# Kernel tuning notes

Measured on AMD Instinct MI355X. Metric: run time of the kernel, lower is better.

Reference implementation:

```python
import jax, jax.numpy as jnp
import numpy as np

B, D, H, C, K = 16384, 128, 4, 64, 16  # nodes, feat dim, heads, out per head, top-k
NEG_SLOPE = 0.2
NEG_INF = -1e9


def setup_inputs() -> dict:
    key = jax.random.key(0)
    ks = jax.random.split(key, 7)
    s = 1.0 / np.sqrt(D)
    return {
        "x": jax.random.normal(ks[0], (B, D), jnp.float32),
        "W_l": jax.random.normal(ks[1], (D, H * C), jnp.float32) * s,
        "b_l": jnp.zeros((H * C,), jnp.float32),
        "W_r": jax.random.normal(ks[2], (D, H * C), jnp.float32) * s,
        "b_r": jnp.zeros((H * C,), jnp.float32),
        "att": jax.random.normal(ks[3], (H, C), jnp.float32) * (1.0 / np.sqrt(C)),
        "bias": jnp.zeros((H * C,), jnp.float32),
        "k": K,
    }


def reference(x, W_l, b_l, W_r, b_r, att, bias, k):
    Bn, Dn = x.shape
    scale = 1.0 / np.sqrt(Dn)
    # dense similarity + top-k graph build (softmax is monotone, so top-k of
    # scaled logits equals top-k of softmax probs)
    attn = (x @ x.T) * scale                      # [B, B]
    _, idx = jax.lax.top_k(attn, k)               # [B, k]

    # edges: node b -> its top-k similar nodes (adj[b, idx[b]] = 1)
    src = jnp.repeat(jnp.arange(Bn), k)           # [B*k]
    dst = idx.reshape(-1)                          # [B*k]
    # GATv2Conv removes self loops then adds exactly one per node
    valid = src != dst
    self_idx = jnp.arange(Bn)
    src = jnp.concatenate([src, self_idx])
    dst = jnp.concatenate([dst, self_idx])
    valid = jnp.concatenate([valid, jnp.ones((Bn,), bool)])  # [E], E = B*(k+1)

    # GATv2: x_l = lin_l(x) for source, x_r = lin_r(x) for target
    x_l = (x @ W_l + b_l).reshape(Bn, H, C)
    x_r = (x @ W_r + b_r).reshape(Bn, H, C)

    msg = x_l[src]                                 # [E, H, C] source features
    s = jax.nn.leaky_relu(msg + x_r[dst], NEG_SLOPE)
    score = jnp.einsum('ehc,hc->eh', s, att)       # [E, H]
    score = jnp.where(valid[:, None], score, NEG_INF)

    # segment softmax over edges grouped by target node
    m = jax.ops.segment_max(score, dst, num_segments=Bn)        # [B, H]
    ex = jnp.exp(score - m[dst]) * valid[:, None].astype(score.dtype)
    denom = jax.ops.segment_sum(ex, dst, num_segments=Bn)       # [B, H]
    alpha = ex / denom[dst]                                     # [E, H]

    out = jax.ops.segment_sum(alpha[:, :, None] * msg, dst, num_segments=Bn)
    return out.reshape(Bn, H * C) + bias
```

## Files before the change

kernel.cpp:

```cpp
#include <hip/hip_runtime.h>
#include <math.h>

#define BN 16384
#define DK 128
#define HN 4
#define CN 64
#define HC 256
#define TK 16
#define CAP 512

#define GSPLIT 16
#define GSPAN  1024
#define GBC    128
#define GNT    (GSPAN / GBC)

#define NSTRIP 2
#define SCOLS (BN / NSTRIP)
#define RPB 64
#define CT 64

typedef float4 f4;
typedef __attribute__((ext_vector_type(8))) short short8;
typedef __attribute__((ext_vector_type(4))) float f32x4;

__device__ __forceinline__ unsigned bf_rne(float f) {
  unsigned u = __float_as_uint(f);
  u += 0x7fffu + ((u >> 16) & 1u);
  return u >> 16;
}

__device__ __forceinline__ unsigned fmap(float f) {
  unsigned b = __float_as_uint(f);
  return (b & 0x80000000u) ? ~b : (b | 0x80000000u);
}

__device__ __forceinline__ void gload16(const unsigned short* g,
                                        unsigned short* l) {
  __builtin_amdgcn_global_load_lds(
      (const __attribute__((address_space(1))) unsigned int*)g,
      (__attribute__((address_space(3))) unsigned int*)l, 16, 0, 0);
}

__global__ __launch_bounds__(256) void k_init(int* deg, int* cur,
                                              unsigned* gmaxu) {
  int i = blockIdx.x * 256 + threadIdx.x;
  if (i < BN) { deg[i] = 1; cur[i] = 0; }
  if (i < BN * 16) gmaxu[i] = 0u;
}

__global__ __launch_bounds__(256) void k_lin(const float* __restrict__ x,
    const float* __restrict__ Wl, const float* __restrict__ bl,
    const float* __restrict__ Wr, const float* __restrict__ br,
    float* __restrict__ xl, float* __restrict__ xr) {
  __shared__ __align__(16) float xst[DK][16];
  int tid = threadIdx.x;
  int r0 = blockIdx.x * 16;
  for (int i = 0; i < 2; ++i) {
    int s = tid + i * 256;
    int r = s >> 5, kq = s & 31;
    f4 v = *(const f4*)&x[(size_t)(r0 + r) * DK + kq * 4];
    xst[kq*4+0][r] = v.x; xst[kq*4+1][r] = v.y;
    xst[kq*4+2][r] = v.z; xst[kq*4+3][r] = v.w;
  }
  __syncthreads();
  float al[16], ar[16];
  #pragma unroll
  for (int r = 0; r < 16; ++r) { al[r] = 0.f; ar[r] = 0.f; }
  for (int k = 0; k < DK; ++k) {
    float wl = Wl[k * HC + tid];
    float wr = Wr[k * HC + tid];
    float xv[16];
    *(f4*)&xv[0]  = *(const f4*)&xst[k][0];
    *(f4*)&xv[4]  = *(const f4*)&xst[k][4];
    *(f4*)&xv[8]  = *(const f4*)&xst[k][8];
    *(f4*)&xv[12] = *(const f4*)&xst[k][12];
    #pragma unroll
    for (int r = 0; r < 16; ++r) { al[r] += xv[r] * wl; ar[r] += xv[r] * wr; }
  }
  float bbl = bl[tid], bbr = br[tid];
  #pragma unroll
  for (int r = 0; r < 16; ++r) {
    xl[(size_t)(r0 + r) * HC + tid] = al[r] + bbl;
    xr[(size_t)(r0 + r) * HC + tid] = ar[r] + bbr;
  }
}

__global__ __launch_bounds__(256) void k_cvt(const float* __restrict__ x,
                                             unsigned short* __restrict__ xbf) {
  size_t base = (size_t)(blockIdx.x * 256 + threadIdx.x) * 8;
  f4 a = *(const f4*)&x[base];
  f4 b = *(const f4*)&x[base + 4];
  uint4 o;
  o.x = bf_rne(a.x) | (bf_rne(a.y) << 16);
  o.y = bf_rne(a.z) | (bf_rne(a.w) << 16);
  o.z = bf_rne(b.x) | (bf_rne(b.y) << 16);
  o.w = bf_rne(b.z) | (bf_rne(b.w) << 16);
  *(uint4*)&xbf[base] = o;
}

template <int MODE>
__global__ __launch_bounds__(512) void k_gemm_t(
    const unsigned short* __restrict__ xbf, unsigned* __restrict__ gmaxu,
    const unsigned* __restrict__ tau_u, int* __restrict__ cnt,
    int* __restrict__ cand) {
  __shared__ __align__(16) unsigned short As[128 * DK];
  __shared__ __align__(16) unsigned short Bs0[128 * DK];
  __shared__ __align__(16) unsigned short Bs1[128 * DK];
  __shared__ float red[4][128];
  int tid = threadIdx.x;
  int q0 = blockIdx.y * 128;
  int c0 = blockIdx.x * GSPAN;
  int lane = tid & 63;
  int wid = tid >> 6;
  int wm = wid & 1, wn = wid >> 1;
  int tq = lane & 15, th = lane >> 4;

  int soff[4];
  #pragma unroll
  for (int i = 0; i < 4; ++i) {
    int slot = tid + i * 512;
    int row = slot >> 4, c8 = slot & 15;
    soff[i] = row * DK + ((c8 ^ (row & 7)) * 8);
  }
  #pragma unroll
  for (int i = 0; i < 4; ++i)
    gload16(&xbf[(size_t)q0 * DK + soff[i]], &As[(tid + i * 512) * 8]);
  #pragma unroll
  for (int i = 0; i < 4; ++i)
    gload16(&xbf[(size_t)c0 * DK + soff[i]], &Bs0[(tid + i * 512) * 8]);
  __syncthreads();

  short8 af[4][4];
  #pragma unroll
  for (int m = 0; m < 4; ++m) {
    int ra = 64 * wm + 16 * m + tq;
    #pragma unroll
    for (int ks = 0; ks < 4; ++ks)
      af[m][ks] = *(const short8*)&As[ra * DK + (((ks*4+th) ^ (ra & 7)) * 8)];
  }

  float gmx[4][4];
  float tauf[4][4];
  if constexpr (MODE == 0) {
    #pragma unroll
    for (int m = 0; m < 4; ++m)
      #pragma unroll
      for (int r = 0; r < 4; ++r) gmx[m][r] = -3.0e38f;
  } else {
    #pragma unroll
    for (int m = 0; m < 4; ++m)
      #pragma unroll
      for (int r = 0; r < 4; ++r) {
        unsigned tu = tau_u[q0 + 64*wm + 16*m + 4*th + r];
        tauf[m][r] = __uint_as_float(
            (tu >= 0x80000000u) ? (tu ^ 0x80000000u) : ~tu);
      }
  }

  if constexpr (MODE == 0) {
    unsigned short* Bc = Bs0;
    unsigned short* Bn = Bs1;
    for (int t = 0; t < GNT; ++t) {
      if (t + 1 < GNT) {
        size_t gb = (size_t)(c0 + (t + 1) * GBC) * DK;
        #pragma unroll
        for (int i = 0; i < 4; ++i)
          gload16(&xbf[gb + soff[i]], &Bn[(tid + i * 512) * 8]);
      }
      short8 bfr[2][4];
      #pragma unroll
      for (int n = 0; n < 2; ++n) {
        int rb = 32 * wn + 16 * n + tq;
        #pragma unroll
        for (int ks = 0; ks < 4; ++ks)
          bfr[n][ks] = *(const short8*)&Bc[rb * DK +
                          (((ks*4+th) ^ (rb & 7)) * 8)];
      }
      f32x4 acc[4][2];
      #pragma unroll
      for (int m = 0; m < 4; ++m)
        #pragma unroll
        for (int n = 0; n < 2; ++n) {
          acc[m][n][0] = 0.f; acc[m][n][1] = 0.f;
          acc[m][n][2] = 0.f; acc[m][n][3] = 0.f;
        }
      #pragma unroll
      for (int ks = 0; ks < 4; ++ks)
        #pragma unroll
        for (int m = 0; m < 4; ++m)
          #pragma unroll
          for (int n = 0; n < 2; ++n)
            acc[m][n] = __builtin_amdgcn_mfma_f32_16x16x32_bf16(
                af[m][ks], bfr[n][ks], acc[m][n], 0, 0, 0);
      #pragma unroll
      for (int m = 0; m < 4; ++m)
        #pragma unroll
        for (int r = 0; r < 4; ++r)
          gmx[m][r] = fmaxf(gmx[m][r], fmaxf(acc[m][0][r], acc[m][1][r]));
      __syncthreads();
      unsigned short* tb = Bc; Bc = Bn; Bn = tb;
    }
    #pragma unroll
    for (int m = 0; m < 4; ++m)
      #pragma unroll
      for (int r = 0; r < 4; ++r) {
        float v = gmx[m][r];
        #pragma unroll
        for (int w = 1; w < 16; w <<= 1) v = fmaxf(v, __shfl_xor(v, w, 64));
        if (tq == 0) red[wn][64*wm + 16*m + 4*th + r] = v;
      }
    __syncthreads();
    if (tid < 128) {
      float v = fmaxf(fmaxf(red[0][tid], red[1][tid]),
                      fmaxf(red[2][tid], red[3][tid]));
      gmaxu[(q0 + tid) * 16 + blockIdx.x] = fmap(v);
    }
  } else {
    unsigned hm[GNT];
    #pragma unroll
    for (int i = 0; i < GNT; ++i) hm[i] = 0u;
    #pragma unroll
    for (int t = 0; t < GNT; ++t) {
      unsigned short* Bc = (t & 1) ? Bs1 : Bs0;
      unsigned short* Bn = (t & 1) ? Bs0 : Bs1;
      if (t + 1 < GNT) {
        size_t gb = (size_t)(c0 + (t + 1) * GBC) * DK;
        #pragma unroll
        for (int i = 0; i < 4; ++i)
          gload16(&xbf[gb + soff[i]], &Bn[(tid + i * 512) * 8]);
      }
      short8 bfr[2][4];
      #pragma unroll
      for (int n = 0; n < 2; ++n) {
        int rb = 32 * wn + 16 * n + tq;
        #pragma unroll
        for (int ks = 0; ks < 4; ++ks)
          bfr[n][ks] = *(const short8*)&Bc[rb * DK +
                          (((ks*4+th) ^ (rb & 7)) * 8)];
      }
      f32x4 acc[4][2];
      #pragma unroll
      for (int m = 0; m < 4; ++m)
        #pragma unroll
        for (int n = 0; n < 2; ++n) {
          acc[m][n][0] = 0.f; acc[m][n][1] = 0.f;
          acc[m][n][2] = 0.f; acc[m][n][3] = 0.f;
        }
      #pragma unroll
      for (int ks = 0; ks < 4; ++ks)
        #pragma unroll
        for (int m = 0; m < 4; ++m)
          #pragma unroll
          for (int n = 0; n < 2; ++n)
            acc[m][n] = __builtin_amdgcn_mfma_f32_16x16x32_bf16(
                af[m][ks], bfr[n][ks], acc[m][n], 0, 0, 0);
      unsigned mm = 0;
      #pragma unroll
      for (int m = 0; m < 4; ++m)
        #pragma unroll
        for (int r = 0; r < 4; ++r)
          #pragma unroll
          for (int n = 0; n < 2; ++n)
            mm |= (acc[m][n][r] >= tauf[m][r])
                      ? (1u << ((m << 3) | (r << 1) | n)) : 0u;
      hm[t] = mm;
      __syncthreads();
    }
    #pragma unroll
    for (int t = 0; t < GNT; ++t) {
      unsigned mm = hm[t];
      while (mm) {
        int b = __ffs(mm) - 1;
        mm &= mm - 1;
        int m = b >> 3, r = (b >> 1) & 3, n = b & 1;
        int row = q0 + 64*wm + 16*m + 4*th + r;
        int col = c0 + t * GBC + 32*wn + 16*n + tq;
        int slot = atomicAdd(&cnt[row], 1);
        if (slot < CAP) cand[(size_t)row * CAP + slot] = col;
      }
    }
  }
}

__global__ __launch_bounds__(256) void k_tau(const unsigned* __restrict__ gmaxu,
    unsigned* __restrict__ tau_u, int* __restrict__ cnt) {
  int row = blockIdx.x * 256 + threadIdx.x;
  unsigned t = 0xFFFFFFFFu;
  #pragma unroll
  for (int g = 0; g < 16; ++g) t = min(t, gmaxu[row * 16 + g]);
  tau_u[row] = t;
  cnt[row] = 0;
}

__global__ __launch_bounds__(256, 4) void k_exact(const float* __restrict__ x,
    const int* __restrict__ cand, const int* __restrict__ cnt,
    int* __restrict__ idx) {
  __shared__ __align__(16) float arow[4][DK];
  int lane = threadIdx.x & 63, wid = threadIdx.x >> 6;
  int row = blockIdx.x * 4 + wid;
  int n = cnt[row];
  if (lane < 32)
    *(f4*)&arow[wid][lane * 4] = *(const f4*)&x[(size_t)row * DK + lane * 4];
  __syncthreads();
  if (n > CAP) return;
  const f4* as = (const f4*)&arow[wid][0];

  if (n <= 64) {
    bool ok = lane < n;
    int col = ok ? cand[(size_t)row * CAP + lane] : row;
    const f4* b4 = (const f4*)&x[(size_t)col * DK];
    f4 pre[8];
    #pragma unroll
    for (int q = 0; q < 8; ++q) pre[q] = b4[q * 4];
    float t = 0.f;
    #pragma unroll
    for (int k = 0; k < 32; ++k) {
      f4 a = as[k];
      f4 b = ((k & 3) == 0) ? pre[k >> 2] : b4[k];
      t = fmaf(a.x, b.x, t); t = fmaf(a.y, b.y, t);
      t = fmaf(a.z, b.z, t); t = fmaf(a.w, b.w, t);
    }
    float sv = ok ? t : -3.0e38f;
    int cc = ok ? col : 0x7fffffff;
    int rk = 0;
    for (int l = 0; l < 64; ++l) {
      float vj = __shfl(sv, l, 64);
      int   cj = __shfl(cc, l, 64);
      rk += (vj > sv || (vj == sv && cj < cc)) ? 1 : 0;
    }
    if (ok && rk < TK) idx[(size_t)row * TK + rk] = cc;
  } else {
    int NCH = (n + 63) >> 6;
    float sv[8]; int cc[8]; int rk[8];
    #pragma unroll
    for (int p = 0; p < 8; ++p) {
      sv[p] = -3.0e38f; cc[p] = 0x7fffffff; rk[p] = 0;
    }
    #pragma unroll
    for (int p = 0; p < 8; ++p) {
      if (p < NCH) {
        int i = p * 64 + lane;
        bool ok = i < n;
        int col = ok ? cand[(size_t)row * CAP + i] : row;
        const f4* b4 = (const f4*)&x[(size_t)col * DK];
        f4 pre[8];
        #pragma unroll
        for (int q = 0; q < 8; ++q) pre[q] = b4[q * 4];
        float t = 0.f;
        #pragma unroll
        for (int k = 0; k < 32; ++k) {
          f4 a = as[k];
          f4 b = ((k & 3) == 0) ? pre[k >> 2] : b4[k];
          t = fmaf(a.x, b.x, t); t = fmaf(a.y, b.y, t);
          t = fmaf(a.z, b.z, t); t = fmaf(a.w, b.w, t);
        }
        if (ok) { sv[p] = t; cc[p] = col; }
      }
    }
    #pragma unroll
    for (int q = 0; q < 8; ++q) {
      if (q < NCH) {
        for (int l = 0; l < 64; ++l) {
          float vj = __shfl(sv[q], l, 64);
          int   cj = __shfl(cc[q], l, 64);
          #pragma unroll
          for (int p = 0; p < 8; ++p)
            rk[p] += (vj > sv[p] || (vj == sv[p] && cj < cc[p])) ? 1 : 0;
        }
      }
    }
    #pragma unroll
    for (int p = 0; p < 8; ++p) {
      int i = p * 64 + lane;
      if (p < NCH && i < n && rk[p] < TK) idx[(size_t)row * TK + rk[p]] = cc[p];
    }
  }
}

__global__ __launch_bounds__(256) void k_exact_of(const float* __restrict__ x,
    const int* __restrict__ cnt, int* __restrict__ idx) {
  int lane = threadIdx.x & 63, wid = threadIdx.x >> 6;
  int row = blockIdx.x * 4 + wid;
  if (cnt[row] <= CAP) return;
  const f4* a4 = (const f4*)&x[(size_t)row * DK];
  float bv[16]; int bc[16];
  #pragma unroll
  for (int i = 0; i < 16; ++i) { bv[i] = -3.0e38f; bc[i] = 0x7fffffff; }
  for (int c = lane; c < BN; c += 64) {
    const f4* b4 = (const f4*)&x[(size_t)c * DK];
    float s = 0.f;
    #pragma unroll
    for (int k = 0; k < 32; ++k) {
      f4 a = a4[k], b = b4[k];
      s = fmaf(a.x, b.x, s); s = fmaf(a.y, b.y, s);
      s = fmaf(a.z, b.z, s); s = fmaf(a.w, b.w, s);
    }
    if (s > bv[15] || (s == bv[15] && c < bc[15])) {
      bv[15] = s; bc[15] = c;
      #pragma unroll
      for (int i = 15; i > 0; --i) {
        bool sw = bv[i] > bv[i-1] || (bv[i] == bv[i-1] && bc[i] < bc[i-1]);
        if (sw) {
          float tv = bv[i]; bv[i] = bv[i-1]; bv[i-1] = tv;
          int tc = bc[i]; bc[i] = bc[i-1]; bc[i-1] = tc;
        }
      }
    }
  }
  for (int t = 0; t < TK; ++t) {
    float mv = bv[0]; int mc = bc[0];
    #pragma unroll
    for (int w = 1; w < 64; w <<= 1) {
      float ov = __shfl_xor(mv, w, 64);
      int   oc = __shfl_xor(mc, w, 64);
      if (ov > mv || (ov == mv && oc < mc)) { mv = ov; mc = oc; }
    }
    if (bv[0] == mv && bc[0] == mc) {
      idx[(size_t)row * TK + t] = mc;
      #pragma unroll
      for (int i = 0; i < 15; ++i) { bv[i] = bv[i+1]; bc[i] = bc[i+1]; }
      bv[15] = -3.0e38f; bc[15] = 0x7fffffff;
    }
  }
}

__global__ __launch_bounds__(256) void k_sim(const float* __restrict__ x,
    int* __restrict__ candC) {
  __shared__ __align__(16) float At[DK][RPB];
  __shared__ __align__(16) float Bt[CT][DK];
  int tid = threadIdx.x;
  int rowblk = blockIdx.x & 255;
  int strip  = blockIdx.x >> 8;
  int r0 = rowblk * RPB;
  int tx = tid & 15, ty = tid >> 4;
  int lane = tid & 63;
  int gbase = lane & 48;
  for (int i = 0; i < 8; ++i) {
    int s = tid + i * 256;
    int r = s >> 5, kq = s & 31;
    f4 v = *(const f4*)&x[(size_t)(r0 + r) * DK + kq * 4];
    At[kq*4+0][r] = v.x; At[kq*4+1][r] = v.y;
    At[kq*4+2][r] = v.z; At[kq*4+3][r] = v.w;
  }
  float listV[4]; int listC[4];
  #pragma unroll
  for (int rr = 0; rr < 4; ++rr) { listV[rr] = -3.0e38f; listC[rr] = 0; }
  __syncthreads();
  for (int ct = 0; ct < SCOLS / CT; ++ct) {
    int c0 = strip * SCOLS + ct * CT;
    for (int i = 0; i < 8; ++i) {
      int s = tid + i * 256;
      int c = s >> 5, kq = s & 31;
      f4 v = *(const f4*)&x[(size_t)(c0 + c) * DK + kq * 4];
      ((f4*)&Bt[c][0])[kq ^ (c & 7)] = v;
    }
    __syncthreads();
    float acc[4][4];
    #pragma unroll
    for (int a = 0; a < 4; ++a)
      #pragma unroll
      for (int b = 0; b < 4; ++b) acc[a][b] = 0.f;
    #pragma unroll 2
    for (int k4 = 0; k4 < 32; ++k4) {
      float ta[4][4], tb[4][4];
      #pragma unroll
      for (int j = 0; j < 4; ++j)
        *(f4*)&ta[j][0] = *(const f4*)&At[k4*4 + j][ty*4];
      #pragma unroll
      for (int jj = 0; jj < 4; ++jj) {
        int c = tx + 16*jj;
        *(f4*)&tb[jj][0] = ((const f4*)&Bt[c][0])[k4 ^ (c & 7)];
      }
      #pragma unroll
      for (int rr = 0; rr < 4; ++rr)
        #pragma unroll
        for (int jj = 0; jj < 4; ++jj)
          acc[rr][jj] += ta[0][rr]*tb[jj][0] + ta[1][rr]*tb[jj][1]
                       + ta[2][rr]*tb[jj][2] + ta[3][rr]*tb[jj][3];
    }
    float tau[4];
    #pragma unroll
    for (int rr = 0; rr < 4; ++rr) tau[rr] = __shfl(listV[rr], 15, 16);
    #pragma unroll
    for (int rr = 0; rr < 4; ++rr) {
      #pragma unroll
      for (int jj = 0; jj < 4; ++jj) {
        float v = acc[rr][jj];
        unsigned long long bal = __ballot(v > tau[rr]);
        unsigned bits = (unsigned)((bal >> gbase) & 0xffffULL);
        while (bits) {
          int l = __ffs(bits) - 1;
          float vb = __shfl(v, l, 16);
          int colb = c0 + l + 16*jj;
          unsigned long long g2 = __ballot(listV[rr] > vb);
          int cnt2 = __popc((unsigned)((g2 >> gbase) & 0xffffULL));
          float sV = __shfl_up(listV[rr], 1, 16);
          int   sC = __shfl_up(listC[rr], 1, 16);
          if (tx == cnt2)      { listV[rr] = vb; listC[rr] = colb; }
          else if (tx > cnt2)  { listV[rr] = sV; listC[rr] = sC; }
          bits &= bits - 1;
        }
      }
    }
    __syncthreads();
  }
  #pragma unroll
  for (int rr = 0; rr < 4; ++rr) {
    int row = r0 + ty * 4 + rr;
    candC[row * (NSTRIP * TK) + strip * TK + tx] = listC[rr];
  }
}

__global__ __launch_bounds__(256) void k_rescore(const float* __restrict__ x,
    const int* __restrict__ candC, int* __restrict__ idx) {
  int lane = threadIdx.x & 63;
  int wid  = threadIdx.x >> 6;
  int half = lane >> 5;
  int ci   = lane & 31;
  int row  = (blockIdx.x * 4 + wid) * 2 + half;
  int col  = candC[row * (NSTRIP * TK) + ci];
  const f4* a4 = (const f4*)&x[(size_t)row * DK];
  const f4* b4 = (const f4*)&x[(size_t)col * DK];
  float s = 0.f;
  #pragma unroll
  for (int k = 0; k < 32; ++k) {
    f4 a = a4[k], b = b4[k];
    s = fmaf(a.x, b.x, s);
    s = fmaf(a.y, b.y, s);
    s = fmaf(a.z, b.z, s);
    s = fmaf(a.w, b.w, s);
  }
  int rank = 0;
  #pragma unroll
  for (int j = 0; j < 32; ++j) {
    float vj = __shfl(s, j, 32);
    int   cj = __shfl(col, j, 32);
    if (vj > s || (vj == s && cj < col)) rank++;
  }
  if (rank < TK) idx[row * TK + rank] = col;
}

__global__ __launch_bounds__(256) void k_count(const int* __restrict__ idx,
                                               int* __restrict__ deg) {
  int i = blockIdx.x * 256 + threadIdx.x;
  int b = i >> 4;
  int t = idx[i];
  if (t != b) atomicAdd(&deg[t], 1);
}

__global__ __launch_bounds__(1024) void k_scan(const int* __restrict__ deg,
                                               int* __restrict__ off) {
  __shared__ int sdat[1024];
  int tid = threadIdx.x;
  int carry = 0;
  for (int ch = 0; ch < BN / 1024; ++ch) {
    int i = ch * 1024 + tid;
    int v = deg[i];
    sdat[tid] = v;
    __syncthreads();
    for (int o = 1; o < 1024; o <<= 1) {
      int t = (tid >= o) ? sdat[tid - o] : 0;
      __syncthreads();
      sdat[tid] += t;
      __syncthreads();
    }
    off[i] = sdat[tid] - v + carry;
    int tot = sdat[1023];
    __syncthreads();
    carry += tot;
  }
  if (tid == 0) off[BN] = carry;
}

__global__ __launch_bounds__(256) void k_fill(const int* __restrict__ idx,
    const int* __restrict__ off, int* __restrict__ cur, int* __restrict__ csr) {
  int i = blockIdx.x * 256 + threadIdx.x;
  if (i >= BN * (TK + 1)) return;
  int b = i / (TK + 1);
  int j = i - b * (TK + 1);
  int t;
  if (j < TK) { t = idx[b * TK + j]; if (t == b) return; }
  else t = b;
  int p = atomicAdd(&cur[t], 1);
  csr[off[t] + p] = b;
}

__global__ __launch_bounds__(256) void k_aggr(const float* __restrict__ xl,
    const float* __restrict__ xr, const float* __restrict__ att,
    const float* __restrict__ bias, const int* __restrict__ off,
    const int* __restrict__ csr, float* __restrict__ out) {
  int t = blockIdx.x;
  int tid = threadIdx.x;
  int o0 = off[t], o1 = off[t + 1];
  float xrv = xr[(size_t)t * HC + tid];
  float av = att[tid];
  float m = -3.0e38f, den = 0.f, acc = 0.f;
  for (int e = o0; e < o1; ++e) {
    int s = csr[e];
    float xlv = xl[(size_t)s * HC + tid];
    float z = xlv + xrv;
    z = (z > 0.f) ? z : 0.2f * z;
    float sc = z * av;
    #pragma unroll
    for (int w = 1; w < 64; w <<= 1) sc += __shfl_xor(sc, w, 64);
    if (sc > m) {
      float r = __expf(m - sc);
      den *= r; acc *= r; m = sc;
    }
    float p = __expf(sc - m);
    den += p;
    acc += p * xlv;
  }
  out[(size_t)t * HC + tid] = acc / den + bias[tid];
}

extern "C" void kernel_launch(void* const* d_in, const int* in_sizes, int n_in,
                              void* d_out, int out_size, void* d_ws, size_t ws_size,
                              hipStream_t stream) {
  const float* x   = (const float*)d_in[0];
  const float* Wl  = (const float*)d_in[1];
  const float* bl  = (const float*)d_in[2];
  const float* Wr  = (const float*)d_in[3];
  const float* br  = (const float*)d_in[4];
  const float* att = (const float*)d_in[5];
  const float* bias= (const float*)d_in[6];
  float* out = (float*)d_out;

  const size_t need =
      (size_t)BN*HC*4*2
    + (size_t)BN*DK*2
    + (size_t)BN*16*4
    + (size_t)BN*4
    + (size_t)BN*4
    + (size_t)BN*CAP*4
    + (size_t)BN*TK*4
    + (size_t)BN*4*3 + 64
    + (size_t)BN*(TK+1)*4;

  if (ws_size >= need) {
    char* p = (char*)d_ws;
    float* xl = (float*)p;                    p += (size_t)BN*HC*4;
    float* xr = (float*)p;                    p += (size_t)BN*HC*4;
    unsigned short* xbf = (unsigned short*)p; p += (size_t)BN*DK*2;
    unsigned* gmaxu = (unsigned*)p;           p += (size_t)BN*16*4;
    unsigned* tau_u = (unsigned*)p;           p += (size_t)BN*4;
    int* cnt = (int*)p;                       p += (size_t)BN*4;
    int* cand = (int*)p;                      p += (size_t)BN*CAP*4;
    int* idx = (int*)p;                       p += (size_t)BN*TK*4;
    int* deg = (int*)p;                       p += (size_t)BN*4;
    int* off = (int*)p;                       p += (size_t)(BN+1)*4 + 60;
    int* cur = (int*)p;                       p += (size_t)BN*4;
    int* csr = (int*)p;

    hipLaunchKernelGGL(k_init, dim3(BN*16/256), dim3(256), 0, stream,
                       deg, cur, gmaxu);
    hipLaunchKernelGGL(k_lin,  dim3(BN/16),  dim3(256), 0, stream,
                       x, Wl, bl, Wr, br, xl, xr);
    hipLaunchKernelGGL(k_cvt,  dim3(BN*DK/(256*8)), dim3(256), 0, stream, x, xbf);
    hipLaunchKernelGGL((k_gemm_t<0>), dim3(GSPLIT, BN/128), dim3(512), 0, stream,
                       xbf, gmaxu, (const unsigned*)nullptr,
                       (int*)nullptr, (int*)nullptr);
    hipLaunchKernelGGL(k_tau,  dim3(BN/256), dim3(256), 0, stream,
                       gmaxu, tau_u, cnt);
    hipLaunchKernelGGL((k_gemm_t<1>), dim3(GSPLIT, BN/128), dim3(512), 0, stream,
                       xbf, (unsigned*)nullptr, tau_u, cnt, cand);
    hipLaunchKernelGGL(k_exact, dim3(BN/4), dim3(256), 0, stream,
                       x, cand, cnt, idx);
    hipLaunchKernelGGL(k_exact_of, dim3(BN/4), dim3(256), 0, stream,
                       x, cnt, idx);
    hipLaunchKernelGGL(k_count, dim3(BN*TK/256), dim3(256), 0, stream, idx, deg);
    hipLaunchKernelGGL(k_scan,  dim3(1), dim3(1024), 0, stream, deg, off);
    hipLaunchKernelGGL(k_fill,  dim3((BN*(TK+1))/256), dim3(256), 0, stream,
                       idx, off, cur, csr);
    hipLaunchKernelGGL(k_aggr,  dim3(BN), dim3(256), 0, stream,
                       xl, xr, att, bias, off, csr, out);
  } else {
    float* xl    = (float*)d_ws;
    float* xr    = xl + (size_t)BN * HC;
    int* candC   = (int*)(xr + (size_t)BN * HC);
    int* idx     = candC + (size_t)BN * NSTRIP * TK;
    int* deg     = idx + (size_t)BN * TK;
    int* off     = deg + BN;
    int* cur     = off + (BN + 1);
    int* csr     = cur + BN;
    unsigned* gmaxu_dummy = (unsigned*)(csr + (size_t)BN * (TK + 1));

    hipLaunchKernelGGL(k_init,  dim3(BN/256), dim3(256), 0, stream,
                       deg, cur, gmaxu_dummy);
    hipLaunchKernelGGL(k_lin,   dim3(BN/16),  dim3(256), 0, stream,
                       x, Wl, bl, Wr, br, xl, xr);
    hipLaunchKernelGGL(k_sim,   dim3(NSTRIP*(BN/RPB)), dim3(256), 0, stream,
                       x, candC);
    hipLaunchKernelGGL(k_rescore, dim3(BN/8), dim3(256), 0, stream,
                       x, candC, idx);
    hipLaunchKernelGGL(k_count, dim3(BN*TK/256), dim3(256), 0, stream, idx, deg);
    hipLaunchKernelGGL(k_scan,  dim3(1), dim3(1024), 0, stream, deg, off);
    hipLaunchKernelGGL(k_fill,  dim3((BN*(TK+1))/256), dim3(256), 0, stream,
                       idx, off, cur, csr);
    hipLaunchKernelGGL(k_aggr,  dim3(BN), dim3(256), 0, stream,
                       xl, xr, att, bias, off, csr, out);
  }
}
```

Baseline: 700.2 us.

## Split exact candidate rescoring into parallel score and rank kernels

Replaces the per-row exact top-k kernel with two kernels. The first computes exact fp32 dot products for every candidate, one thread per candidate and one block per row, and writes them to a new workspace buffer. The second ranks candidates within a wavefront by pairwise comparison using shuffles. This aims to expose more parallelism in the dot-product phase, at the cost of an extra buffer round trip through memory and a second launch. It only runs when the workspace is large enough, otherwise it falls back to the old kernel.

```diff
diff --git a/kernel.cpp b/kernel.cpp
--- a/kernel.cpp
+++ b/kernel.cpp
@@ -290,6 +290,76 @@
   for (int g = 0; g < 16; ++g) t = min(t, gmaxu[row * 16 + g]);
   tau_u[row] = t;
   cnt[row] = 0;
+}
+
+__global__ __launch_bounds__(512, 4) void k_score(const float* __restrict__ x,
+    const int* __restrict__ cand, const int* __restrict__ cnt,
+    float* __restrict__ svbuf) {
+  __shared__ __align__(16) float arow[DK];
+  int row = blockIdx.x;
+  int i = threadIdx.x;
+  int n = cnt[row];
+  if (i < 32)
+    *(f4*)&arow[i * 4] = *(const f4*)&x[(size_t)row * DK + i * 4];
+  __syncthreads();
+  if (n > CAP || i >= n) return;
+  const f4* as = (const f4*)arow;
+  int col = cand[(size_t)row * CAP + i];
+  const f4* b4 = (const f4*)&x[(size_t)col * DK];
+  f4 pre[8];
+  #pragma unroll
+  for (int q = 0; q < 8; ++q) pre[q] = b4[q * 4];
+  float t = 0.f;
+  #pragma unroll
+  for (int k = 0; k < 32; ++k) {
+    f4 a = as[k];
+    f4 b = ((k & 3) == 0) ? pre[k >> 2] : b4[k];
+    t = fmaf(a.x, b.x, t); t = fmaf(a.y, b.y, t);
+    t = fmaf(a.z, b.z, t); t = fmaf(a.w, b.w, t);
+  }
+  svbuf[(size_t)row * CAP + i] = t;
+}
+
+__global__ __launch_bounds__(256) void k_rank(const float* __restrict__ svbuf,
+    const int* __restrict__ cand, const int* __restrict__ cnt,
+    int* __restrict__ idx) {
+  int lane = threadIdx.x & 63, wid = threadIdx.x >> 6;
+  int row = blockIdx.x * 4 + wid;
+  int n = cnt[row];
+  if (n > CAP) return;
+  int NCH = (n + 63) >> 6;
+  float sv[8]; int cc[8]; int rk[8];
+  #pragma unroll
+  for (int p = 0; p < 8; ++p) {
+    sv[p] = -3.0e38f; cc[p] = 0x7fffffff; rk[p] = 0;
+  }
+  #pragma unroll
+  for (int p = 0; p < 8; ++p) {
+    if (p < NCH) {
+      int i = p * 64 + lane;
+      if (i < n) {
+        sv[p] = svbuf[(size_t)row * CAP + i];
+        cc[p] = cand[(size_t)row * CAP + i];
+      }
+    }
+  }
+  #pragma unroll
+  for (int q = 0; q < 8; ++q) {
+    if (q < NCH) {
+      for (int l = 0; l < 64; ++l) {
+        float vj = __shfl(sv[q], l, 64);
+        int   cj = __shfl(cc[q], l, 64);
+        #pragma unroll
+        for (int p = 0; p < 8; ++p)
+          rk[p] += (vj > sv[p] || (vj == sv[p] && cj < cc[p])) ? 1 : 0;
+      }
+    }
+  }
+  #pragma unroll
+  for (int p = 0; p < 8; ++p) {
+    int i = p * 64 + lane;
+    if (p < NCH && i < n && rk[p] < TK) idx[(size_t)row * TK + rk[p]] = cc[p];
+  }
 }
 
 __global__ __launch_bounds__(256, 4) void k_exact(const float* __restrict__ x,
@@ -636,6 +706,7 @@
     + (size_t)BN*TK*4
     + (size_t)BN*4*3 + 64
     + (size_t)BN*(TK+1)*4;
+  const size_t need2 = need + (size_t)BN*CAP*4;
 
   if (ws_size >= need) {
     char* p = (char*)d_ws;
@@ -650,7 +721,8 @@
     int* deg = (int*)p;                       p += (size_t)BN*4;
     int* off = (int*)p;                       p += (size_t)(BN+1)*4 + 60;
     int* cur = (int*)p;                       p += (size_t)BN*4;
-    int* csr = (int*)p;
+    int* csr = (int*)p;                       p += (size_t)BN*(TK+1)*4;
+    float* svbuf = (float*)p;
 
     hipLaunchKernelGGL(k_init, dim3(BN*16/256), dim3(256), 0, stream,
                        deg, cur, gmaxu);
@@ -664,8 +736,15 @@
                        gmaxu, tau_u, cnt);
     hipLaunchKernelGGL((k_gemm_t<1>), dim3(GSPLIT, BN/128), dim3(512), 0, stream,
                        xbf, (unsigned*)nullptr, tau_u, cnt, cand);
-    hipLaunchKernelGGL(k_exact, dim3(BN/4), dim3(256), 0, stream,
-                       x, cand, cnt, idx);
+    if (ws_size >= need2) {
+      hipLaunchKernelGGL(k_score, dim3(BN), dim3(512), 0, stream,
+                         x, cand, cnt, svbuf);
+      hipLaunchKernelGGL(k_rank,  dim3(BN/4), dim3(256), 0, stream,
+                         svbuf, cand, cnt, idx);
+    } else {
+      hipLaunchKernelGGL(k_exact, dim3(BN/4), dim3(256), 0, stream,
+                         x, cand, cnt, idx);
+    }
     hipLaunchKernelGGL(k_exact_of, dim3(BN/4), dim3(256), 0, stream,
                        x, cnt, idx);
     hipLaunchKernelGGL(k_count, dim3(BN*TK/256), dim3(256), 0, stream, idx, deg);
```

New measurement: 668.5 us. 1.05x faster.
